# Kernel tuning notes

Measured on AMD Instinct MI355X. Metric: run time of the kernel, lower is better.

The kernel has to match this reference:

```python
import jax, jax.numpy as jnp
import numpy as np

B, T, C = 2, 2048, 2048
N_HEADS, HEAD_DIM = 16, 128
THETA = 10000.0


def _rope_cos_sin(T, dim, theta=THETA):
    inv_freq = 1.0 / (theta ** (jnp.arange(0, dim, 2, dtype=jnp.float32) / dim))  # (dim/2,)
    t = jnp.arange(T, dtype=jnp.float32)
    freqs = jnp.outer(t, inv_freq)  # (T, dim/2)
    return jnp.cos(freqs), jnp.sin(freqs)


def _apply_rope(x, cos, sin):
    # x: (B, H, T, D); cos/sin: (T, D/2) -> broadcast over B, H
    xr = x[..., 0::2]
    xi = x[..., 1::2]
    or_ = xr * cos - xi * sin
    oi_ = xr * sin + xi * cos
    return jnp.stack([or_, oi_], axis=-1).reshape(x.shape)


def setup_inputs() -> dict:
    key = jax.random.key(0)
    ks = jax.random.split(key, 5)
    scale = 1.0 / np.sqrt(C)
    x = jax.random.normal(ks[0], (B, T, C), dtype=jnp.float32)
    wq = jax.random.normal(ks[1], (C, N_HEADS * HEAD_DIM), dtype=jnp.float32) * scale
    wk = jax.random.normal(ks[2], (C, N_HEADS * HEAD_DIM), dtype=jnp.float32) * scale
    wv = jax.random.normal(ks[3], (C, N_HEADS * HEAD_DIM), dtype=jnp.float32) * scale
    wo = jax.random.normal(ks[4], (N_HEADS * HEAD_DIM, C), dtype=jnp.float32) * scale
    mask = jnp.tril(jnp.ones((T, T), dtype=bool))[None, None]  # causal (1,1,T,T)
    return {"x": x, "mask": mask, "wq": wq, "wk": wk, "wv": wv, "wo": wo}


def reference(x, mask, wq, wk, wv, wo):
    Bx, Tx, Cx = x.shape
    cos, sin = _rope_cos_sin(Tx, HEAD_DIM)
    # projections -> (B, H, T, D)
    def proj(w):
        return (x @ w).reshape(Bx, Tx, N_HEADS, HEAD_DIM).transpose(0, 2, 1, 3)
    q = _apply_rope(proj(wq), cos, sin)
    k = _apply_rope(proj(wk), cos, sin)
    v = proj(wv)
    scores = jnp.einsum("bhqd,bhkd->bhqk", q, k) / jnp.sqrt(jnp.float32(HEAD_DIM))
    scores = jnp.where(mask, scores, -jnp.inf)
    attn = jax.nn.softmax(scores, axis=-1)
    out = jnp.einsum("bhqk,bhkd->bhqd", attn, v)
    out = out.transpose(0, 2, 1, 3).reshape(Bx, Tx, Cx)
    return out @ wo
```

## Files before the change

### kernel.cpp

```cpp
#include <hip/hip_runtime.h>
#include <stdint.h>

#define B_  2
#define T_  2048
#define C_  2048
#define NH  16
#define HD  128
#define M_  (B_*T_)

typedef unsigned short ushort_t;
typedef unsigned int uint;
typedef __attribute__((ext_vector_type(8))) short short8;
typedef __attribute__((ext_vector_type(4))) float f32x4;
typedef __attribute__((ext_vector_type(16))) float f32x16;

#if __has_builtin(__builtin_amdgcn_exp2f)
#define EXP2 __builtin_amdgcn_exp2f
#else
#define EXP2 exp2f
#endif

__device__ inline ushort_t f2b(float f) {
  union { float f; unsigned u; } x; x.f = f;
  unsigned r = (x.u + 0x7fffu + ((x.u >> 16) & 1u)) >> 16;
  return (ushort_t)r;
}
__device__ inline float b2f(ushort_t b) {
  union { unsigned u; float f; } x; x.u = ((unsigned)b) << 16;
  return x.f;
}
__device__ inline uint cvtpk(float lo, float hi) {
  uint d;
  asm("v_cvt_pk_bf16_f32 %0, %1, %2" : "=v"(d) : "v"(lo), "v"(hi));
  return d;
}
__device__ inline void pl32swap(uint& a, uint& b) {
  asm volatile("v_permlane32_swap_b32 %0, %1" : "+v"(a), "+v"(b));
}
__device__ inline void gload_lds16(const void* g, void* l) {
  __builtin_amdgcn_global_load_lds((const __attribute__((address_space(1))) void*)g,
                                   (__attribute__((address_space(3))) void*)l, 16, 0, 0);
}

__global__ __launch_bounds__(256) void cvt_f32_bf16(const float* __restrict__ in,
                                                    ushort_t* __restrict__ out, int n4) {
  int i = blockIdx.x * 256 + threadIdx.x;
  if (i >= n4) return;
  float4 v = ((const float4*)in)[i];
  unsigned long long pk = (unsigned long long)f2b(v.x)
                        | ((unsigned long long)f2b(v.y) << 16)
                        | ((unsigned long long)f2b(v.z) << 32)
                        | ((unsigned long long)f2b(v.w) << 48);
  ((unsigned long long*)out)[i] = pk;
}

template<int FROM_F32>
__global__ __launch_bounds__(256) void transpose_to_bf16(const void* __restrict__ inv,
                                                         ushort_t* __restrict__ out,
                                                         int rows, int cols) {
  __shared__ __align__(16) ushort_t tile[64][72];
  const int t = threadIdx.x;
  const int br = blockIdx.y * 64, bc = blockIdx.x * 64;
  if (FROM_F32) {
    const float* in = (const float*)inv;
    const int vc = t & 15, r0 = t >> 4;
#pragma unroll
    for (int i = 0; i < 4; i++) {
      int row = r0 + 16 * i;
      float4 v = *(const float4*)&in[(size_t)(br + row) * cols + bc + vc * 4];
      tile[row][vc * 4 + 0] = f2b(v.x);
      tile[row][vc * 4 + 1] = f2b(v.y);
      tile[row][vc * 4 + 2] = f2b(v.z);
      tile[row][vc * 4 + 3] = f2b(v.w);
    }
  } else {
    const ushort_t* in = (const ushort_t*)inv;
    const int vc = t & 7, r0 = t >> 3;
#pragma unroll
    for (int i = 0; i < 2; i++) {
      int row = r0 + 32 * i;
      short8 v = *(const short8*)&in[(size_t)(br + row) * cols + bc + vc * 8];
#pragma unroll
      for (int j = 0; j < 8; j++) tile[row][vc * 8 + j] = (ushort_t)v[j];
    }
  }
  __syncthreads();
  const int oc = t >> 2;
#pragma unroll
  for (int s2 = 0; s2 < 2; s2++) {
    int seg = (t & 3) + 4 * s2;
    short8 w;
#pragma unroll
    for (int j = 0; j < 8; j++) w[j] = (short)tile[seg * 8 + j][oc];
    *(short8*)&out[(size_t)(bc + oc) * rows + br + seg * 8] = w;
  }
}

__global__ __launch_bounds__(256) void rope_table(float* __restrict__ cs, float* __restrict__ sn) {
  int i = blockIdx.x * 256 + threadIdx.x;
  int tt = i >> 6, f = i & 63;
  float inv = powf(10000.0f, -(float)(2 * f) / 128.0f);
  float ang = (float)tt * inv;
  cs[i] = cosf(ang);
  sn[i] = sinf(ang);
}

__global__ __launch_bounds__(256) void rope_apply(ushort_t* __restrict__ Q, ushort_t* __restrict__ K,
                                                  const float* __restrict__ cs,
                                                  const float* __restrict__ sn) {
  int i = blockIdx.x * 256 + threadIdx.x;
  int row = i >> 8, g = i & 255;
  int tt = row & (T_ - 1);
  int fb = (g * 4) & 63;
  f32x4 cv = *(const f32x4*)&cs[(tt << 6) + fb];
  f32x4 sv = *(const f32x4*)&sn[(tt << 6) + fb];
  size_t idx = ((size_t)row << 11) + (size_t)g * 8;
  short8 q = *(const short8*)&Q[idx];
  short8 k = *(const short8*)&K[idx];
#pragma unroll
  for (int j = 0; j < 4; j++) {
    float c = cv[j], s = sv[j];
    float qr = b2f((ushort_t)q[2 * j]), qi = b2f((ushort_t)q[2 * j + 1]);
    q[2 * j]     = (short)f2b(qr * c - qi * s);
    q[2 * j + 1] = (short)f2b(qr * s + qi * c);
    float kr = b2f((ushort_t)k[2 * j]), ki = b2f((ushort_t)k[2 * j + 1]);
    k[2 * j]     = (short)f2b(kr * c - ki * s);
    k[2 * j + 1] = (short)f2b(kr * s + ki * c);
  }
  *(short8*)&Q[idx] = q;
  *(short8*)&K[idx] = k;
}

template<int OUTF32>
__global__ __launch_bounds__(512, 2) void gemm_bt256(const ushort_t* __restrict__ A,
                                                     const ushort_t* __restrict__ Bt0,
                                                     const ushort_t* __restrict__ Bt1,
                                                     const ushort_t* __restrict__ Bt2,
                                                     void* __restrict__ O0, void* __restrict__ O1,
                                                     void* __restrict__ O2, int N, int K) {
  extern __shared__ __align__(16) ushort_t lds[];
  const int z = blockIdx.z;
  const ushort_t* Bt = (z == 0) ? Bt0 : (z == 1) ? Bt1 : Bt2;
  void* Ov = (z == 0) ? O0 : (z == 1) ? O1 : O2;
  const int tid = threadIdx.x;
  const int lane = tid & 63, wave = tid >> 6;
  const int lr = lane & 15, lg = lane >> 4;
  const int wm = wave >> 2, wn = wave & 3;
  const int swz = lr & 7;
  const int bm = blockIdx.y, bn = blockIdx.x;
  const ushort_t* Ap = A + (size_t)bm * 256 * K;
  const ushort_t* Bp = Bt + (size_t)bn * 256 * K;
  const int NT = K >> 6;

  f32x4 acc[8][4] = {};

  auto stage8 = [&](int k0, int base) {
#pragma unroll
    for (int i = 0; i < 4; i++) {
      int idx = i * 512 + wave * 64 + lane;
      int row = idx >> 3;
      int c = (idx & 7) ^ (row & 7);
      gload_lds16(Ap + (size_t)row * K + k0 + c * 8,
                  &lds[(size_t)base + (size_t)(i * 512 + wave * 64) * 8]);
    }
#pragma unroll
    for (int i = 0; i < 4; i++) {
      int idx = i * 512 + wave * 64 + lane;
      int row = idx >> 3;
      int c = (idx & 7) ^ (row & 7);
      gload_lds16(Bp + (size_t)row * K + k0 + c * 8,
                  &lds[(size_t)base + 16384 + (size_t)(i * 512 + wave * 64) * 8]);
    }
  };

  stage8(0, 0);

  for (int t = 0; t < NT; t++) {
    __builtin_amdgcn_s_barrier();
    if (t + 1 < NT) {
      stage8((t + 1) << 6, ((t + 1) & 1) * 32768);
      asm volatile("s_waitcnt vmcnt(8)" ::: "memory");
    } else {
      asm volatile("s_waitcnt vmcnt(0)" ::: "memory");
    }
    __builtin_amdgcn_s_barrier();
    const int abase = (t & 1) * 32768, bbase = abase + 16384;
    __builtin_amdgcn_s_setprio(1);
#pragma unroll
    for (int kk = 0; kk < 2; kk++) {
      short8 af[8], bf[4];
#pragma unroll
      for (int mf = 0; mf < 8; mf++)
        af[mf] = *(const short8*)&lds[abase + (wm * 128 + mf * 16 + lr) * 64 +
                                      (((kk * 4) + lg) ^ swz) * 8];
#pragma unroll
      for (int nf = 0; nf < 4; nf++)
        bf[nf] = *(const short8*)&lds[bbase + (wn * 64 + nf * 16 + lr) * 64 +
                                      (((kk * 4) + lg) ^ swz) * 8];
#pragma unroll
      for (int mf = 0; mf < 8; mf++)
#pragma unroll
        for (int nf = 0; nf < 4; nf++)
          acc[mf][nf] = __builtin_amdgcn_mfma_f32_16x16x32_bf16(af[mf], bf[nf], acc[mf][nf], 0, 0, 0);
    }
    __builtin_amdgcn_s_setprio(0);
  }

  const int row0 = bm * 256 + wm * 128 + lg * 4;
  const int col0 = bn * 256 + wn * 64 + lr;
  if (OUTF32) {
    float* O = (float*)Ov;
#pragma unroll
    for (int mf = 0; mf < 8; mf++)
#pragma unroll
      for (int nf = 0; nf < 4; nf++)
#pragma unroll
        for (int r = 0; r < 4; r++)
          O[(size_t)(row0 + mf * 16 + r) * N + col0 + nf * 16] = acc[mf][nf][r];
  } else {
    ushort_t* O = (ushort_t*)Ov;
#pragma unroll
    for (int mf = 0; mf < 8; mf++)
#pragma unroll
      for (int nf = 0; nf < 4; nf++)
#pragma unroll
        for (int r = 0; r < 4; r++)
          O[(size_t)(row0 + mf * 16 + r) * N + col0 + nf * 16] = f2b(acc[mf][nf][r]);
  }
}

__global__ __launch_bounds__(64) void flash_attn3(const ushort_t* __restrict__ Q,
                                                  const ushort_t* __restrict__ K,
                                                  const ushort_t* __restrict__ Vt,
                                                  ushort_t* __restrict__ AO) {
  int flat = blockIdx.x;
  int swz = (flat & 7) * 128 + (flat >> 3);
  const int bh = swz >> 5, widx = swz & 31;
  const int b = bh >> 4, h = bh & 15;
  const int lane = threadIdx.x & 63;
  const int col = lane & 31, hi = lane >> 5, hioff = 4 * hi;
  const ushort_t* Qb = Q + (size_t)b * T_ * C_ + (size_t)h * HD;
  const ushort_t* Kb = K + (size_t)b * T_ * C_ + (size_t)h * HD;
  const ushort_t* Vb = Vt + (size_t)bh * (size_t)HD * T_;
  const float sc = 0.12754245f;

#pragma unroll 1
  for (int ph = 0; ph < 2; ph++) {
    const int tile = ph ? (63 - widx) : widx;
    const int q0 = tile * 32;
    const int qcol = q0 + col;
    short8 qf[8];
#pragma unroll
    for (int db = 0; db < 8; db++)
      qf[db] = *(const short8*)&Qb[(size_t)qcol * C_ + db * 16 + hi * 8];

    f32x16 o0 = {}, o1 = {}, o2 = {}, o3 = {};
    float m = -1e30f, l = 0.f;

    short8 kf[8];
#pragma unroll
    for (int db = 0; db < 8; db++)
      kf[db] = *(const short8*)&Kb[(size_t)col * C_ + db * 16 + hi * 8];

#pragma unroll 1
    for (int k0 = 0; k0 <= q0; k0 += 32) {
      f32x16 s = {};
#pragma unroll
      for (int db = 0; db < 8; db++)
        s = __builtin_amdgcn_mfma_f32_32x32x16_bf16(kf[db], qf[db], s, 0, 0, 0);
      if (k0 + 32 <= q0) {
#pragma unroll
        for (int db = 0; db < 8; db++)
          kf[db] = *(const short8*)&Kb[(size_t)(k0 + 32 + col) * C_ + db * 16 + hi * 8];
      }
      short8 va[4][2];
#pragma unroll
      for (int dblk = 0; dblk < 4; dblk++)
#pragma unroll
        for (int j = 0; j < 2; j++)
          va[dblk][j] = *(const short8*)&Vb[(size_t)(dblk * 32 + col) * T_ + k0 + j * 16 + hi * 8];

      const bool domask = (k0 + 31 > q0);
      if (domask) {
#pragma unroll
        for (int r = 0; r < 16; r++) {
          int krow = k0 + ((r & 3) + 8 * (r >> 2)) + hioff;
          float v = s[r] * sc;
          s[r] = (krow > qcol) ? -1e30f : v;
        }
      } else {
#pragma unroll
        for (int r = 0; r < 16; r++) s[r] = s[r] * sc;
      }
      float tm = s[0];
#pragma unroll
      for (int r = 1; r < 16; r++) tm = fmaxf(tm, s[r]);
      tm = fmaxf(tm, __shfl_xor(tm, 32, 64));
      if (!__all(tm <= m + 8.0f)) {
        float mn = fmaxf(m, tm);
        float corr = EXP2(m - mn);
        m = mn;
        l *= corr;
#pragma unroll
        for (int r = 0; r < 16; r++) { o0[r] *= corr; o1[r] *= corr; o2[r] *= corr; o3[r] *= corr; }
      }
#pragma unroll
      for (int r = 0; r < 16; r++) s[r] = EXP2(s[r] - m);
      float rs = s[0];
#pragma unroll
      for (int r = 1; r < 16; r++) rs += s[r];
      rs += __shfl_xor(rs, 32, 64);
      l += rs;
      uint c0 = cvtpk(s[0], s[1]),  c1 = cvtpk(s[2], s[3]);
      uint c2 = cvtpk(s[4], s[5]),  c3 = cvtpk(s[6], s[7]);
      uint c4 = cvtpk(s[8], s[9]),  c5 = cvtpk(s[10], s[11]);
      uint c6 = cvtpk(s[12], s[13]), c7 = cvtpk(s[14], s[15]);
      pl32swap(c0, c2); pl32swap(c1, c3);
      pl32swap(c4, c6); pl32swap(c5, c7);
      union { uint u[4]; short8 v; } pb0, pb1;
      pb0.u[0] = c0; pb0.u[1] = c1; pb0.u[2] = c2; pb0.u[3] = c3;
      pb1.u[0] = c4; pb1.u[1] = c5; pb1.u[2] = c6; pb1.u[3] = c7;
      o0 = __builtin_amdgcn_mfma_f32_32x32x16_bf16(va[0][0], pb0.v, o0, 0, 0, 0);
      o1 = __builtin_amdgcn_mfma_f32_32x32x16_bf16(va[1][0], pb0.v, o1, 0, 0, 0);
      o2 = __builtin_amdgcn_mfma_f32_32x32x16_bf16(va[2][0], pb0.v, o2, 0, 0, 0);
      o3 = __builtin_amdgcn_mfma_f32_32x32x16_bf16(va[3][0], pb0.v, o3, 0, 0, 0);
      o0 = __builtin_amdgcn_mfma_f32_32x32x16_bf16(va[0][1], pb1.v, o0, 0, 0, 0);
      o1 = __builtin_amdgcn_mfma_f32_32x32x16_bf16(va[1][1], pb1.v, o1, 0, 0, 0);
      o2 = __builtin_amdgcn_mfma_f32_32x32x16_bf16(va[2][1], pb1.v, o2, 0, 0, 0);
      o3 = __builtin_amdgcn_mfma_f32_32x32x16_bf16(va[3][1], pb1.v, o3, 0, 0, 0);
    }
    float inv = 1.0f / l;
    size_t rowbase = (size_t)(b * T_ + qcol) * C_ + h * HD;
#pragma unroll
    for (int r = 0; r < 16; r++) {
      int d = (r & 3) + 8 * (r >> 2) + hioff;
      AO[rowbase + d]      = f2b(o0[r] * inv);
      AO[rowbase + 32 + d] = f2b(o1[r] * inv);
      AO[rowbase + 64 + d] = f2b(o2[r] * inv);
      AO[rowbase + 96 + d] = f2b(o3[r] * inv);
    }
  }
}

extern "C" void kernel_launch(void* const* d_in, const int* in_sizes, int n_in,
                              void* d_out, int out_size, void* d_ws, size_t ws_size,
                              hipStream_t stream) {
  const float* x  = (const float*)d_in[0];
  const float* wq = (const float*)d_in[2];
  const float* wk = (const float*)d_in[3];
  const float* wv = (const float*)d_in[4];
  const float* wo = (const float*)d_in[5];

  char* ws = (char*)d_ws;
  size_t off = 0;
  auto alloc = [&](size_t bytes) { char* p = ws + off; off += (bytes + 255) & ~255ull; return p; };
  ushort_t* Qb  = (ushort_t*)alloc((size_t)M_ * C_ * 2);
  ushort_t* Kb  = (ushort_t*)alloc((size_t)M_ * C_ * 2);
  ushort_t* Vb  = (ushort_t*)alloc((size_t)M_ * C_ * 2);
  ushort_t* Vtb = (ushort_t*)alloc((size_t)M_ * C_ * 2);
  ushort_t* xb  = (ushort_t*)alloc((size_t)M_ * C_ * 2);
  ushort_t* AO  = xb;
  ushort_t* wqt = (ushort_t*)alloc((size_t)C_ * C_ * 2);
  ushort_t* wkt = (ushort_t*)alloc((size_t)C_ * C_ * 2);
  ushort_t* wvt = (ushort_t*)alloc((size_t)C_ * C_ * 2);
  ushort_t* wot = (ushort_t*)alloc((size_t)C_ * C_ * 2);
  float* cs = (float*)alloc((size_t)T_ * 64 * 4);
  float* sn = (float*)alloc((size_t)T_ * 64 * 4);

  cvt_f32_bf16<<<(M_ * C_ / 4 + 255) / 256, 256, 0, stream>>>(x, xb, M_ * C_ / 4);
  dim3 tg(C_ / 64, C_ / 64);
  transpose_to_bf16<1><<<tg, 256, 0, stream>>>(wq, wqt, C_, C_);
  transpose_to_bf16<1><<<tg, 256, 0, stream>>>(wk, wkt, C_, C_);
  transpose_to_bf16<1><<<tg, 256, 0, stream>>>(wv, wvt, C_, C_);
  transpose_to_bf16<1><<<tg, 256, 0, stream>>>(wo, wot, C_, C_);
  rope_table<<<T_ * 64 / 256, 256, 0, stream>>>(cs, sn);
  gemm_bt256<0><<<dim3(C_ / 256, M_ / 256, 3), 512, 131072, stream>>>(
      xb, wqt, wkt, wvt, Qb, Kb, Vb, C_, C_);
  rope_apply<<<M_ * C_ / 8 / 256, 256, 0, stream>>>(Qb, Kb, cs, sn);
  for (int b = 0; b < B_; b++)
    transpose_to_bf16<0><<<dim3(T_ / 64, T_ / 64), 256, 0, stream>>>(
        Vb + (size_t)b * T_ * C_, Vtb + (size_t)b * T_ * C_, T_, C_);
  flash_attn3<<<dim3(B_ * NH * 32), 64, 0, stream>>>(Qb, Kb, Vtb, AO);
  gemm_bt256<1><<<dim3(C_ / 256, M_ / 256, 1), 512, 131072, stream>>>(
      AO, wot, wot, wot, d_out, d_out, d_out, C_, C_);
  (void)in_sizes; (void)n_in; (void)out_size; (void)ws_size;
}
```

Measured before the change: 481.4 us.

## Shrink GEMM tile to 256x128 and use triple-buffered LDS pipeline

The projection GEMMs now use 256x128 output tiles, with a 4x2 wave layout that gives each wave a 64x64 sub-tile. The LDS staging moves from double to triple buffering, with loads issued two K-steps ahead. This doubles the number of blocks, which helps fill the GPU, and hides global-load latency better. The costs are lower arithmetic intensity per block, more LDS per block (144KB, which likely allows only one block per CU), and an extra barrier per iteration.

```diff
diff --git a/kernel.cpp b/kernel.cpp
--- a/kernel.cpp
+++ b/kernel.cpp
@@ -132,12 +132,12 @@
 }
 
 template<int OUTF32>
-__global__ __launch_bounds__(512, 2) void gemm_bt256(const ushort_t* __restrict__ A,
-                                                     const ushort_t* __restrict__ Bt0,
-                                                     const ushort_t* __restrict__ Bt1,
-                                                     const ushort_t* __restrict__ Bt2,
-                                                     void* __restrict__ O0, void* __restrict__ O1,
-                                                     void* __restrict__ O2, int N, int K) {
+__global__ __launch_bounds__(512, 2) void gemm_bt3(const ushort_t* __restrict__ A,
+                                                   const ushort_t* __restrict__ Bt0,
+                                                   const ushort_t* __restrict__ Bt1,
+                                                   const ushort_t* __restrict__ Bt2,
+                                                   void* __restrict__ O0, void* __restrict__ O1,
+                                                   void* __restrict__ O2, int N, int K) {
   extern __shared__ __align__(16) ushort_t lds[];
   const int z = blockIdx.z;
   const ushort_t* Bt = (z == 0) ? Bt0 : (z == 1) ? Bt1 : Bt2;
@@ -145,73 +145,70 @@
   const int tid = threadIdx.x;
   const int lane = tid & 63, wave = tid >> 6;
   const int lr = lane & 15, lg = lane >> 4;
-  const int wm = wave >> 2, wn = wave & 3;
+  const int wm = wave >> 1, wn = wave & 1;
   const int swz = lr & 7;
   const int bm = blockIdx.y, bn = blockIdx.x;
   const ushort_t* Ap = A + (size_t)bm * 256 * K;
-  const ushort_t* Bp = Bt + (size_t)bn * 256 * K;
+  const ushort_t* Bp = Bt + (size_t)bn * 128 * K;
   const int NT = K >> 6;
 
-  f32x4 acc[8][4] = {};
-
-  auto stage8 = [&](int k0, int base) {
+  f32x4 acc[4][4] = {};
+
+  auto stage = [&](int k0, int buf) {
+    const int base = buf * 24576;
 #pragma unroll
     for (int i = 0; i < 4; i++) {
-      int idx = i * 512 + wave * 64 + lane;
+      int idx = i * 512 + tid;
       int row = idx >> 3;
       int c = (idx & 7) ^ (row & 7);
-      gload_lds16(Ap + (size_t)row * K + k0 + c * 8,
-                  &lds[(size_t)base + (size_t)(i * 512 + wave * 64) * 8]);
-    }
-#pragma unroll
-    for (int i = 0; i < 4; i++) {
-      int idx = i * 512 + wave * 64 + lane;
+      gload_lds16(Ap + (size_t)row * K + k0 + c * 8, &lds[(size_t)(base + idx * 8)]);
+    }
+#pragma unroll
+    for (int i = 0; i < 2; i++) {
+      int idx = i * 512 + tid;
       int row = idx >> 3;
       int c = (idx & 7) ^ (row & 7);
-      gload_lds16(Bp + (size_t)row * K + k0 + c * 8,
-                  &lds[(size_t)base + 16384 + (size_t)(i * 512 + wave * 64) * 8]);
+      gload_lds16(Bp + (size_t)row * K + k0 + c * 8, &lds[(size_t)(base + 16384 + idx * 8)]);
     }
   };
 
-  stage8(0, 0);
+  stage(0, 0);
+  stage(64, 1);
 
   for (int t = 0; t < NT; t++) {
+    if (t + 2 < NT) stage((t + 2) << 6, (t + 2) % 3);
+    if (t < NT - 2)       asm volatile("s_waitcnt vmcnt(12)" ::: "memory");
+    else if (t == NT - 2) asm volatile("s_waitcnt vmcnt(6)"  ::: "memory");
+    else                  asm volatile("s_waitcnt vmcnt(0)"  ::: "memory");
     __builtin_amdgcn_s_barrier();
-    if (t + 1 < NT) {
-      stage8((t + 1) << 6, ((t + 1) & 1) * 32768);
-      asm volatile("s_waitcnt vmcnt(8)" ::: "memory");
-    } else {
-      asm volatile("s_waitcnt vmcnt(0)" ::: "memory");
-    }
-    __builtin_amdgcn_s_barrier();
-    const int abase = (t & 1) * 32768, bbase = abase + 16384;
+    const int abase = (t % 3) * 24576, bbase = abase + 16384;
     __builtin_amdgcn_s_setprio(1);
 #pragma unroll
     for (int kk = 0; kk < 2; kk++) {
-      short8 af[8], bf[4];
-#pragma unroll
-      for (int mf = 0; mf < 8; mf++)
-        af[mf] = *(const short8*)&lds[abase + (wm * 128 + mf * 16 + lr) * 64 +
-                                      (((kk * 4) + lg) ^ swz) * 8];
+      short8 af[4], bf[4];
+      const int ch = ((kk * 4 + lg) ^ swz) * 8;
+#pragma unroll
+      for (int mf = 0; mf < 4; mf++)
+        af[mf] = *(const short8*)&lds[abase + (wm * 64 + mf * 16 + lr) * 64 + ch];
 #pragma unroll
       for (int nf = 0; nf < 4; nf++)
-        bf[nf] = *(const short8*)&lds[bbase + (wn * 64 + nf * 16 + lr) * 64 +
-                                      (((kk * 4) + lg) ^ swz) * 8];
-#pragma unroll
-      for (int mf = 0; mf < 8; mf++)
+        bf[nf] = *(const short8*)&lds[bbase + (wn * 64 + nf * 16 + lr) * 64 + ch];
+#pragma unroll
+      for (int mf = 0; mf < 4; mf++)
 #pragma unroll
         for (int nf = 0; nf < 4; nf++)
           acc[mf][nf] = __builtin_amdgcn_mfma_f32_16x16x32_bf16(af[mf], bf[nf], acc[mf][nf], 0, 0, 0);
     }
     __builtin_amdgcn_s_setprio(0);
-  }
-
-  const int row0 = bm * 256 + wm * 128 + lg * 4;
-  const int col0 = bn * 256 + wn * 64 + lr;
+    __builtin_amdgcn_s_barrier();
+  }
+
+  const int row0 = bm * 256 + wm * 64 + lg * 4;
+  const int col0 = bn * 128 + wn * 64 + lr;
   if (OUTF32) {
     float* O = (float*)Ov;
 #pragma unroll
-    for (int mf = 0; mf < 8; mf++)
+    for (int mf = 0; mf < 4; mf++)
 #pragma unroll
       for (int nf = 0; nf < 4; nf++)
 #pragma unroll
@@ -220,7 +217,7 @@
   } else {
     ushort_t* O = (ushort_t*)Ov;
 #pragma unroll
-    for (int mf = 0; mf < 8; mf++)
+    for (int mf = 0; mf < 4; mf++)
 #pragma unroll
       for (int nf = 0; nf < 4; nf++)
 #pragma unroll
@@ -374,14 +371,14 @@
   transpose_to_bf16<1><<<tg, 256, 0, stream>>>(wv, wvt, C_, C_);
   transpose_to_bf16<1><<<tg, 256, 0, stream>>>(wo, wot, C_, C_);
   rope_table<<<T_ * 64 / 256, 256, 0, stream>>>(cs, sn);
-  gemm_bt256<0><<<dim3(C_ / 256, M_ / 256, 3), 512, 131072, stream>>>(
+  gemm_bt3<0><<<dim3(C_ / 128, M_ / 256, 3), 512, 147456, stream>>>(
       xb, wqt, wkt, wvt, Qb, Kb, Vb, C_, C_);
   rope_apply<<<M_ * C_ / 8 / 256, 256, 0, stream>>>(Qb, Kb, cs, sn);
   for (int b = 0; b < B_; b++)
     transpose_to_bf16<0><<<dim3(T_ / 64, T_ / 64), 256, 0, stream>>>(
         Vb + (size_t)b * T_ * C_, Vtb + (size_t)b * T_ * C_, T_, C_);
   flash_attn3<<<dim3(B_ * NH * 32), 64, 0, stream>>>(Qb, Kb, Vtb, AO);
-  gemm_bt256<1><<<dim3(C_ / 256, M_ / 256, 1), 512, 131072, stream>>>(
+  gemm_bt3<1><<<dim3(C_ / 128, M_ / 256, 1), 512, 147456, stream>>>(
       AO, wot, wot, wot, d_out, d_out, d_out, C_, C_);
   (void)in_sizes; (void)n_in; (void)out_size; (void)ws_size;
 }
```

Result: faster. 456.7 us (-5.1%).
